# Performance work log

Measured on AMD Instinct MI355X. Metric: run time of the kernel, lower is better.

## Reference

```python
import jax, jax.numpy as jnp
import numpy as np

N = 50000      # nodes
E = 1600000    # edges (avg degree 32)
D_IN = 32
D_EF = 16
D_H = 64
D_MSG = 32
D_UP = 32


def setup_inputs() -> dict:
    key = jax.random.key(0)
    ks = jax.random.split(key, 10)
    s = 0.05
    return {
        "x": jax.random.normal(ks[0], (N, D_IN), dtype=jnp.float32),
        "degrees": jax.random.uniform(ks[1], (N, 1), dtype=jnp.float32),
        "edge_features": jax.random.normal(ks[2], (E, D_EF), dtype=jnp.float32),
        "W1m": jax.random.normal(ks[3], (2 * D_IN + D_EF, D_H), dtype=jnp.float32) * s,
        "b1m": jnp.zeros((D_H,), dtype=jnp.float32),
        "W2m": jax.random.normal(ks[4], (D_H, D_MSG), dtype=jnp.float32) * s,
        "b2m": jnp.zeros((D_MSG,), dtype=jnp.float32),
        "W1u": jax.random.normal(ks[5], (D_IN + D_MSG, D_H), dtype=jnp.float32) * s,
        "b1u": jnp.zeros((D_H,), dtype=jnp.float32),
        "W2u": jax.random.normal(ks[6], (D_H, D_UP), dtype=jnp.float32) * s,
        "b2u": jnp.zeros((D_UP,), dtype=jnp.float32),
        "edge_index": jax.random.randint(ks[7], (2, E), 0, N, dtype=jnp.int64),
    }


def mlp2(h, W1, b1, W2, b2):
    return jax.nn.relu(h @ W1 + b1) @ W2 + b2


def reference(x, degrees, edge_features, W1m, b1m, W2m, b2m, W1u, b1u, W2u, b2u, edge_index):
    # flow = 'source_to_target': select=1 -> i = targets = edge_index[1],
    # j = sources = edge_index[0]; sparse.sum over dim 0 aggregates per target.
    src = edge_index[0]
    dst = edge_index[1]
    x_i = x[dst]                                  # [E, D_IN] target features
    x_j = x[src]                                  # [E, D_IN] source features
    msg_in = jnp.concatenate([x_i, x_j, edge_features], axis=-1)  # [E, 2*D_IN+D_EF]
    msgs = mlp2(msg_in, W1m, b1m, W2m, b2m)       # [E, D_MSG]
    agg = jax.ops.segment_sum(msgs, dst, num_segments=x.shape[0])  # [N, D_MSG]
    upd_in = jnp.concatenate([x, agg], axis=-1)   # [N, D_IN+D_MSG]
    return mlp2(upd_in, W1u, b1u, W2u, b2u)       # [N, D_UP]
```

## Files before the change

### kernel.cpp

```cpp
#include <hip/hip_runtime.h>
#include <hip/hip_bf16.h>

#define D_IN  32
#define D_EF  16
#define D_H   64
#define D_MSG 32
#define D_UP  32

typedef __fp16 v2h __attribute__((ext_vector_type(2)));

__device__ __forceinline__ unsigned bf16pair(float a, float b) {
    unsigned ua = __float_as_uint(a);
    ua = (ua + 0x7fffu + ((ua >> 16) & 1u)) >> 16;
    unsigned ub = __float_as_uint(b);
    ub = (ub + 0x7fffu + ((ub >> 16) & 1u)) >> 16;
    return ua | (ub << 16);
}
__device__ __forceinline__ float bf_lo(unsigned u) { return __uint_as_float(u << 16); }
__device__ __forceinline__ float bf_hi(unsigned u) { return __uint_as_float(u & 0xffff0000u); }

__global__ __launch_bounds__(256) void prep_kernel(
    const float* __restrict__ x,
    const float* __restrict__ W1m,
    const float* __restrict__ b1m,
    const int*   __restrict__ ei,
    float* __restrict__ P1,
    unsigned short* __restrict__ P2b,
    int* __restrict__ deg,
    int* __restrict__ rank,
    v2h* __restrict__ W1Ep,
    int n_nodes, int n_edges, int NBn, int NBe)
{
    int b = blockIdx.x;

    if (b < NBn) {
        int i = b * 256 + threadIdx.x;
        if (i >= n_nodes) return;

        float xi[D_IN];
        const float4* xp = (const float4*)(x + (size_t)i * D_IN);
#pragma unroll
        for (int k4 = 0; k4 < D_IN / 4; ++k4) {
            float4 v = xp[k4];
            xi[4 * k4 + 0] = v.x; xi[4 * k4 + 1] = v.y;
            xi[4 * k4 + 2] = v.z; xi[4 * k4 + 3] = v.w;
        }
        {
            float acc[D_H];
#pragma unroll
            for (int j = 0; j < D_H; ++j) acc[j] = b1m[j];
            for (int k = 0; k < D_IN; ++k) {
                float xv = xi[k];
                const float* wr = W1m + (size_t)k * D_H;
#pragma unroll
                for (int j = 0; j < D_H; ++j) acc[j] += xv * wr[j];
            }
            float4* o = (float4*)(P1 + (size_t)i * D_H);
#pragma unroll
            for (int j4 = 0; j4 < D_H / 4; ++j4)
                o[j4] = make_float4(acc[4 * j4], acc[4 * j4 + 1],
                                    acc[4 * j4 + 2], acc[4 * j4 + 3]);
        }
        {
            float acc[D_H];
#pragma unroll
            for (int j = 0; j < D_H; ++j) acc[j] = 0.0f;
            for (int k = 0; k < D_IN; ++k) {
                float xv = xi[k];
                const float* wr = W1m + (size_t)(k + D_IN) * D_H;
#pragma unroll
                for (int j = 0; j < D_H; ++j) acc[j] += xv * wr[j];
            }
            uint4* o = (uint4*)(P2b + (size_t)i * D_H);
#pragma unroll
            for (int j8 = 0; j8 < D_H / 8; ++j8) {
                uint4 q;
                q.x = bf16pair(acc[8 * j8 + 0], acc[8 * j8 + 1]);
                q.y = bf16pair(acc[8 * j8 + 2], acc[8 * j8 + 3]);
                q.z = bf16pair(acc[8 * j8 + 4], acc[8 * j8 + 5]);
                q.w = bf16pair(acc[8 * j8 + 6], acc[8 * j8 + 7]);
                o[j8] = q;
            }
        }
    } else if (b < NBn + NBe) {
        int e = (b - NBn) * 256 + threadIdx.x;
        if (e < n_edges)
            rank[e] = atomicAdd(&deg[ei[n_edges + e]], 1);
    } else {
        int t = threadIdx.x;
        const float* W1E = W1m + (size_t)(2 * D_IN) * D_H;
        for (int idx = t; idx < 8 * D_H; idx += 256) {
            int kp = idx >> 6, c = idx & 63;
            W1Ep[idx] = __builtin_amdgcn_cvt_pkrtz(W1E[(2 * kp) * D_H + c],
                                                   W1E[(2 * kp + 1) * D_H + c]);
        }
    }
}

__global__ __launch_bounds__(256) void scan_partials_kernel(
    const int* __restrict__ deg, int* __restrict__ bsum, int n_nodes)
{
    int idx = blockIdx.x * 256 + threadIdx.x;
    int v = (idx < n_nodes) ? deg[idx] : 0;
#pragma unroll
    for (int o = 1; o < 64; o <<= 1) v += __shfl_xor(v, o, 64);
    __shared__ int ws[4];
    int lane = threadIdx.x & 63, w = threadIdx.x >> 6;
    if (lane == 0) ws[w] = v;
    __syncthreads();
    if (threadIdx.x == 0) bsum[blockIdx.x] = ws[0] + ws[1] + ws[2] + ws[3];
}

__global__ __launch_bounds__(256) void scan_blockoffs_kernel(
    const int* __restrict__ bsum, int* __restrict__ boffs, int nb)
{
    __shared__ int sdata[256];
    int t = threadIdx.x;
    sdata[t] = (t < nb) ? bsum[t] : 0;
    __syncthreads();
    for (int off = 1; off < 256; off <<= 1) {
        int u = (t >= off) ? sdata[t - off] : 0;
        __syncthreads();
        sdata[t] += u;
        __syncthreads();
    }
    if (t < nb) boffs[t] = (t > 0) ? sdata[t - 1] : 0;
}

__global__ __launch_bounds__(256) void scan_final_kernel(
    const int* __restrict__ deg, const int* __restrict__ boffs,
    int* __restrict__ offs, int n_nodes)
{
    __shared__ int sdata[256];
    int t = threadIdx.x;
    int idx = blockIdx.x * 256 + t;
    sdata[t] = (idx < n_nodes) ? deg[idx] : 0;
    __syncthreads();
    for (int off = 1; off < 256; off <<= 1) {
        int u = (t >= off) ? sdata[t - off] : 0;
        __syncthreads();
        sdata[t] += u;
        __syncthreads();
    }
    int excl = boffs[blockIdx.x] + ((t > 0) ? sdata[t - 1] : 0);
    if (idx < n_nodes) offs[idx] = excl;
}

__global__ __launch_bounds__(256) void scatter_kernel(
    const int* __restrict__ ei,
    const int* __restrict__ rank,
    const int* __restrict__ offs,
    int2* __restrict__ edges_sorted,
    int n_edges)
{
    int e = blockIdx.x * blockDim.x + threadIdx.x;
    if (e < n_edges) {
        int s = ei[e];
        int d = ei[n_edges + e];
        int pos = offs[d] + rank[e];
        edges_sorted[pos] = make_int2(e, s);
    }
}

__global__ __launch_bounds__(256) void gather_kernel(
    const float* __restrict__ ef,
    const v2h*  __restrict__ W1Ep,
    const float* __restrict__ P1,
    const unsigned short* __restrict__ P2b,
    const int*  __restrict__ deg,
    const int*  __restrict__ offs,
    const int2* __restrict__ edges_sorted,
    float* __restrict__ hagg,
    int n_nodes)
{
    int tid = blockIdx.x * blockDim.x + threadIdx.x;
    int n = tid >> 4;
    int t = tid & 15;
    if (n >= n_nodes) return;

    int start = offs[n];
    int end   = start + deg[n];
    const float* P1n = P1 + (size_t)n * D_H;

    float hacc[D_H];
#pragma unroll
    for (int c = 0; c < D_H; ++c) hacc[c] = 0.0f;

    int i = start + t;
    int s = 0;
    float4 ef0, ef1, ef2, ef3;
    if (i < end) {
        int2 es = edges_sorted[i];
        s = es.y;
        const float4* efp = (const float4*)(ef + (size_t)es.x * D_EF);
        ef0 = efp[0]; ef1 = efp[1]; ef2 = efp[2]; ef3 = efp[3];
    }

    while (i < end) {
        int inext = i + 16;
        int ip = (inext < end) ? inext : i;
        int2 es2 = edges_sorted[ip];
        const float4* efp2 = (const float4*)(ef + (size_t)es2.x * D_EF);
        float4 nf0 = efp2[0], nf1 = efp2[1], nf2 = efp2[2], nf3 = efp2[3];

        v2h efh[D_EF / 2];
        efh[0] = __builtin_amdgcn_cvt_pkrtz(ef0.x, ef0.y);
        efh[1] = __builtin_amdgcn_cvt_pkrtz(ef0.z, ef0.w);
        efh[2] = __builtin_amdgcn_cvt_pkrtz(ef1.x, ef1.y);
        efh[3] = __builtin_amdgcn_cvt_pkrtz(ef1.z, ef1.w);
        efh[4] = __builtin_amdgcn_cvt_pkrtz(ef2.x, ef2.y);
        efh[5] = __builtin_amdgcn_cvt_pkrtz(ef2.z, ef2.w);
        efh[6] = __builtin_amdgcn_cvt_pkrtz(ef3.x, ef3.y);
        efh[7] = __builtin_amdgcn_cvt_pkrtz(ef3.z, ef3.w);

        const float4* p1  = (const float4*)P1n;
        const uint4*  p2u = (const uint4*)(P2b + (size_t)s * D_H);

#pragma unroll
        for (int j = 0; j < D_H / 8; ++j) {
            uint4 b = p2u[j];
            float4 a0 = p1[2 * j], a1 = p1[2 * j + 1];
            float h[8];
            h[0] = a0.x + bf_lo(b.x); h[1] = a0.y + bf_hi(b.x);
            h[2] = a0.z + bf_lo(b.y); h[3] = a0.w + bf_hi(b.y);
            h[4] = a1.x + bf_lo(b.z); h[5] = a1.y + bf_hi(b.z);
            h[6] = a1.z + bf_lo(b.w); h[7] = a1.w + bf_hi(b.w);

#pragma unroll
            for (int kp = 0; kp < D_EF / 2; ++kp) {
                const v2h* wr = W1Ep + kp * D_H + 8 * j;
#pragma unroll
                for (int c8 = 0; c8 < 8; ++c8)
                    h[c8] = __builtin_amdgcn_fdot2(efh[kp], wr[c8], h[c8], false);
            }

#pragma unroll
            for (int c8 = 0; c8 < 8; ++c8) {
                float r = h[c8] > 0.0f ? h[c8] : 0.0f;
                hacc[8 * j + c8] += r;
            }
        }

        i = inext; s = es2.y;
        ef0 = nf0; ef1 = nf1; ef2 = nf2; ef3 = nf3;
    }

    float r1[32];
    {
        const bool up = (t & 8) != 0;
#pragma unroll
        for (int c = 0; c < 32; ++c) {
            float lo = hacc[c]      + __shfl_xor(hacc[c],      8, 16);
            float hi = hacc[c + 32] + __shfl_xor(hacc[c + 32], 8, 16);
            r1[c] = up ? hi : lo;
        }
    }
    float r2[16];
    {
        const bool up = (t & 4) != 0;
#pragma unroll
        for (int c = 0; c < 16; ++c) {
            float lo = r1[c]      + __shfl_xor(r1[c],      4, 16);
            float hi = r1[c + 16] + __shfl_xor(r1[c + 16], 4, 16);
            r2[c] = up ? hi : lo;
        }
    }
    float r3[8];
    {
        const bool up = (t & 2) != 0;
#pragma unroll
        for (int c = 0; c < 8; ++c) {
            float lo = r2[c]     + __shfl_xor(r2[c],     2, 16);
            float hi = r2[c + 8] + __shfl_xor(r2[c + 8], 2, 16);
            r3[c] = up ? hi : lo;
        }
    }
    float r4[4];
    {
        const bool up = (t & 1) != 0;
#pragma unroll
        for (int c = 0; c < 4; ++c) {
            float lo = r3[c]     + __shfl_xor(r3[c],     1, 16);
            float hi = r3[c + 4] + __shfl_xor(r3[c + 4], 1, 16);
            r4[c] = up ? hi : lo;
        }
    }

    ((float4*)(hagg + (size_t)n * D_H))[t] =
        make_float4(r4[0], r4[1], r4[2], r4[3]);
}

__global__ __launch_bounds__(256) void node_upd_kernel(
    const float* __restrict__ x,
    const float* __restrict__ hagg,
    const int*   __restrict__ deg,
    const float* __restrict__ b2m,
    const float* __restrict__ W2m,
    const float* __restrict__ W1u,
    const float* __restrict__ b1u,
    const float* __restrict__ W2u,
    const float* __restrict__ b2u,
    float* __restrict__ out,
    int n_nodes)
{
    int i = blockIdx.x * blockDim.x + threadIdx.x;
    if (i >= n_nodes) return;

    float in[D_IN + D_MSG];
    const float4* xp = (const float4*)(x + (size_t)i * D_IN);
#pragma unroll
    for (int k4 = 0; k4 < D_IN / 4; ++k4) {
        float4 v = xp[k4];
        in[4 * k4 + 0] = v.x; in[4 * k4 + 1] = v.y;
        in[4 * k4 + 2] = v.z; in[4 * k4 + 3] = v.w;
    }

    float dc = (float)deg[i];
#pragma unroll
    for (int m = 0; m < D_MSG; ++m) in[D_IN + m] = dc * b2m[m];

    const float4* hp = (const float4*)(hagg + (size_t)i * D_H);
    for (int j4 = 0; j4 < D_H / 4; ++j4) {
        float4 v = hp[j4];
        const float* w0 = W2m + (size_t)(4 * j4 + 0) * D_MSG;
        const float* w1 = W2m + (size_t)(4 * j4 + 1) * D_MSG;
        const float* w2 = W2m + (size_t)(4 * j4 + 2) * D_MSG;
        const float* w3 = W2m + (size_t)(4 * j4 + 3) * D_MSG;
#pragma unroll
        for (int m = 0; m < D_MSG; ++m)
            in[D_IN + m] += v.x * w0[m] + v.y * w1[m] + v.z * w2[m] + v.w * w3[m];
    }

    float h[D_H];
#pragma unroll
    for (int j = 0; j < D_H; ++j) h[j] = b1u[j];
    for (int k = 0; k < D_IN + D_MSG; ++k) {
        float v = in[k];
        const float* wr = W1u + (size_t)k * D_H;
#pragma unroll
        for (int j = 0; j < D_H; ++j) h[j] += v * wr[j];
    }

    float o[D_UP];
#pragma unroll
    for (int m = 0; m < D_UP; ++m) o[m] = b2u[m];
    for (int j = 0; j < D_H; ++j) {
        float r = h[j] > 0.0f ? h[j] : 0.0f;
        const float* wr = W2u + (size_t)j * D_UP;
#pragma unroll
        for (int m = 0; m < D_UP; ++m) o[m] += r * wr[m];
    }

    float4* op = (float4*)(out + (size_t)i * D_UP);
#pragma unroll
    for (int m4 = 0; m4 < D_UP / 4; ++m4)
        op[m4] = make_float4(o[4 * m4], o[4 * m4 + 1], o[4 * m4 + 2], o[4 * m4 + 3]);
}

extern "C" void kernel_launch(void* const* d_in, const int* in_sizes, int n_in,
                              void* d_out, int out_size, void* d_ws, size_t ws_size,
                              hipStream_t stream) {
    const float* x    = (const float*)d_in[0];
    const float* ef   = (const float*)d_in[2];
    const float* W1m  = (const float*)d_in[3];
    const float* b1m  = (const float*)d_in[4];
    const float* W2m  = (const float*)d_in[5];
    const float* b2m  = (const float*)d_in[6];
    const float* W1u  = (const float*)d_in[7];
    const float* b1u  = (const float*)d_in[8];
    const float* W2u  = (const float*)d_in[9];
    const float* b2u  = (const float*)d_in[10];
    const int*   ei   = (const int*)d_in[11];

    const int n_nodes = in_sizes[0] / D_IN;
    const int n_edges = in_sizes[11] / 2;

    float* out = (float*)d_out;

    const int NBn = (n_nodes + 255) / 256;
    const int NBe = (n_edges + 255) / 256;

    float*          P1  = (float*)d_ws;
    unsigned short* P2b = (unsigned short*)(P1 + (size_t)n_nodes * D_H);
    int2* edges_sorted  = (int2*)(P2b + (size_t)n_nodes * D_H);
    int* deg    = (int*)(edges_sorted + n_edges);
    int* offs   = deg    + n_nodes;
    int* bsum   = offs   + n_nodes;
    int* boffs  = bsum   + NBn;
    v2h* W1Ep   = (v2h*)(boffs + NBn);
    int*   rank = (int*)(W1Ep + 8 * D_H);
    float* hagg = (float*)rank;

    hipMemsetAsync(deg, 0, (size_t)n_nodes * sizeof(int), stream);

    prep_kernel<<<NBn + NBe + 1, 256, 0, stream>>>(
        x, W1m, b1m, ei, P1, P2b, deg, rank, W1Ep,
        n_nodes, n_edges, NBn, NBe);

    scan_partials_kernel<<<NBn, 256, 0, stream>>>(deg, bsum, n_nodes);
    scan_blockoffs_kernel<<<1, 256, 0, stream>>>(bsum, boffs, NBn);
    scan_final_kernel<<<NBn, 256, 0, stream>>>(deg, boffs, offs, n_nodes);

    scatter_kernel<<<NBe, 256, 0, stream>>>(ei, rank, offs, edges_sorted, n_edges);

    {
        long total = (long)n_nodes * 16;
        int grid = (int)((total + 255) / 256);
        gather_kernel<<<grid, 256, 0, stream>>>(ef, W1Ep, P1, P2b,
                                                deg, offs, edges_sorted, hagg,
                                                n_nodes);
    }
    node_upd_kernel<<<NBn, 256, 0, stream>>>(x, hagg, deg, b2m, W2m,
                                             W1u, b1u, W2u, b2u, out, n_nodes);
}
```

Measured before the change: 516.5 us.

## Split gather hidden channels across four waves per node group

Each 256-thread block now handles 4 nodes. Each wavefront covers one 16-column slice of the 64-wide hidden layer, so a thread keeps 16 accumulators instead of 64. The point is to cut register pressure, raise occupancy (launch bounds of 6 waves) and shrink the shuffle reduction. The cost is that every wave re-reads edges_sorted and the edge features, so those reads rise 4x, and the software prefetch of the next edge is gone.

```diff
diff --git a/kernel.cpp b/kernel.cpp
--- a/kernel.cpp
+++ b/kernel.cpp
@@ -162,7 +162,7 @@
     }
 }
 
-__global__ __launch_bounds__(256) void gather_kernel(
+__global__ __launch_bounds__(256, 6) void gather_kernel(
     const float* __restrict__ ef,
     const v2h*  __restrict__ W1Ep,
     const float* __restrict__ P1,
@@ -173,62 +173,66 @@
     float* __restrict__ hagg,
     int n_nodes)
 {
-    int tid = blockIdx.x * blockDim.x + threadIdx.x;
-    int n = tid >> 4;
-    int t = tid & 15;
+    const int lane = threadIdx.x & 63;
+    const int cg   = __builtin_amdgcn_readfirstlane((int)(threadIdx.x >> 6));
+    const int g    = lane >> 4;
+    const int t    = lane & 15;
+    const int n    = blockIdx.x * 4 + g;
     if (n >= n_nodes) return;
 
-    int start = offs[n];
-    int end   = start + deg[n];
-    const float* P1n = P1 + (size_t)n * D_H;
-
-    float hacc[D_H];
-#pragma unroll
-    for (int c = 0; c < D_H; ++c) hacc[c] = 0.0f;
-
-    int i = start + t;
-    int s = 0;
-    float4 ef0, ef1, ef2, ef3;
-    if (i < end) {
+    const int start = offs[n];
+    const int end   = start + deg[n];
+
+    float p1q[16];
+    {
+        const float4* pp = (const float4*)(P1 + (size_t)n * D_H + cg * 16);
+#pragma unroll
+        for (int q = 0; q < 4; ++q) {
+            float4 v = pp[q];
+            p1q[4 * q + 0] = v.x; p1q[4 * q + 1] = v.y;
+            p1q[4 * q + 2] = v.z; p1q[4 * q + 3] = v.w;
+        }
+    }
+
+    const v2h* wbase = W1Ep + 16 * cg;
+
+    float hacc[16];
+#pragma unroll
+    for (int c = 0; c < 16; ++c) hacc[c] = 0.0f;
+
+    for (int i = start + t; i < end; i += 16) {
         int2 es = edges_sorted[i];
-        s = es.y;
         const float4* efp = (const float4*)(ef + (size_t)es.x * D_EF);
-        ef0 = efp[0]; ef1 = efp[1]; ef2 = efp[2]; ef3 = efp[3];
-    }
-
-    while (i < end) {
-        int inext = i + 16;
-        int ip = (inext < end) ? inext : i;
-        int2 es2 = edges_sorted[ip];
-        const float4* efp2 = (const float4*)(ef + (size_t)es2.x * D_EF);
-        float4 nf0 = efp2[0], nf1 = efp2[1], nf2 = efp2[2], nf3 = efp2[3];
+        float4 f0 = efp[0], f1 = efp[1], f2 = efp[2], f3 = efp[3];
+        const uint4* p2u = (const uint4*)(P2b + (size_t)es.y * D_H + cg * 16);
+        uint4 b0 = p2u[0], b1 = p2u[1];
 
         v2h efh[D_EF / 2];
-        efh[0] = __builtin_amdgcn_cvt_pkrtz(ef0.x, ef0.y);
-        efh[1] = __builtin_amdgcn_cvt_pkrtz(ef0.z, ef0.w);
-        efh[2] = __builtin_amdgcn_cvt_pkrtz(ef1.x, ef1.y);
-        efh[3] = __builtin_amdgcn_cvt_pkrtz(ef1.z, ef1.w);
-        efh[4] = __builtin_amdgcn_cvt_pkrtz(ef2.x, ef2.y);
-        efh[5] = __builtin_amdgcn_cvt_pkrtz(ef2.z, ef2.w);
-        efh[6] = __builtin_amdgcn_cvt_pkrtz(ef3.x, ef3.y);
-        efh[7] = __builtin_amdgcn_cvt_pkrtz(ef3.z, ef3.w);
-
-        const float4* p1  = (const float4*)P1n;
-        const uint4*  p2u = (const uint4*)(P2b + (size_t)s * D_H);
-
-#pragma unroll
-        for (int j = 0; j < D_H / 8; ++j) {
-            uint4 b = p2u[j];
-            float4 a0 = p1[2 * j], a1 = p1[2 * j + 1];
+        efh[0] = __builtin_amdgcn_cvt_pkrtz(f0.x, f0.y);
+        efh[1] = __builtin_amdgcn_cvt_pkrtz(f0.z, f0.w);
+        efh[2] = __builtin_amdgcn_cvt_pkrtz(f1.x, f1.y);
+        efh[3] = __builtin_amdgcn_cvt_pkrtz(f1.z, f1.w);
+        efh[4] = __builtin_amdgcn_cvt_pkrtz(f2.x, f2.y);
+        efh[5] = __builtin_amdgcn_cvt_pkrtz(f2.z, f2.w);
+        efh[6] = __builtin_amdgcn_cvt_pkrtz(f3.x, f3.y);
+        efh[7] = __builtin_amdgcn_cvt_pkrtz(f3.z, f3.w);
+
+#pragma unroll
+        for (int jj = 0; jj < 2; ++jj) {
+            uint4 b = jj ? b1 : b0;
             float h[8];
-            h[0] = a0.x + bf_lo(b.x); h[1] = a0.y + bf_hi(b.x);
-            h[2] = a0.z + bf_lo(b.y); h[3] = a0.w + bf_hi(b.y);
-            h[4] = a1.x + bf_lo(b.z); h[5] = a1.y + bf_hi(b.z);
-            h[6] = a1.z + bf_lo(b.w); h[7] = a1.w + bf_hi(b.w);
+            h[0] = p1q[8 * jj + 0] + bf_lo(b.x);
+            h[1] = p1q[8 * jj + 1] + bf_hi(b.x);
+            h[2] = p1q[8 * jj + 2] + bf_lo(b.y);
+            h[3] = p1q[8 * jj + 3] + bf_hi(b.y);
+            h[4] = p1q[8 * jj + 4] + bf_lo(b.z);
+            h[5] = p1q[8 * jj + 5] + bf_hi(b.z);
+            h[6] = p1q[8 * jj + 6] + bf_lo(b.w);
+            h[7] = p1q[8 * jj + 7] + bf_hi(b.w);
 
 #pragma unroll
             for (int kp = 0; kp < D_EF / 2; ++kp) {
-                const v2h* wr = W1Ep + kp * D_H + 8 * j;
+                const v2h* wr = wbase + kp * D_H + 8 * jj;
 #pragma unroll
                 for (int c8 = 0; c8 < 8; ++c8)
                     h[c8] = __builtin_amdgcn_fdot2(efh[kp], wr[c8], h[c8], false);
@@ -237,57 +241,50 @@
 #pragma unroll
             for (int c8 = 0; c8 < 8; ++c8) {
                 float r = h[c8] > 0.0f ? h[c8] : 0.0f;
-                hacc[8 * j + c8] += r;
+                hacc[8 * jj + c8] += r;
             }
         }
-
-        i = inext; s = es2.y;
-        ef0 = nf0; ef1 = nf1; ef2 = nf2; ef3 = nf3;
-    }
-
-    float r1[32];
+    }
+
+    float r1[8];
     {
         const bool up = (t & 8) != 0;
 #pragma unroll
-        for (int c = 0; c < 32; ++c) {
-            float lo = hacc[c]      + __shfl_xor(hacc[c],      8, 16);
-            float hi = hacc[c + 32] + __shfl_xor(hacc[c + 32], 8, 16);
+        for (int c = 0; c < 8; ++c) {
+            float lo = hacc[c]     + __shfl_xor(hacc[c],     8, 16);
+            float hi = hacc[c + 8] + __shfl_xor(hacc[c + 8], 8, 16);
             r1[c] = up ? hi : lo;
         }
     }
-    float r2[16];
+    float r2[4];
     {
         const bool up = (t & 4) != 0;
 #pragma unroll
-        for (int c = 0; c < 16; ++c) {
-            float lo = r1[c]      + __shfl_xor(r1[c],      4, 16);
-            float hi = r1[c + 16] + __shfl_xor(r1[c + 16], 4, 16);
+        for (int c = 0; c < 4; ++c) {
+            float lo = r1[c]     + __shfl_xor(r1[c],     4, 16);
+            float hi = r1[c + 4] + __shfl_xor(r1[c + 4], 4, 16);
             r2[c] = up ? hi : lo;
         }
     }
-    float r3[8];
+    float r3[2];
     {
         const bool up = (t & 2) != 0;
 #pragma unroll
-        for (int c = 0; c < 8; ++c) {
+        for (int c = 0; c < 2; ++c) {
             float lo = r2[c]     + __shfl_xor(r2[c],     2, 16);
-            float hi = r2[c + 8] + __shfl_xor(r2[c + 8], 2, 16);
+            float hi = r2[c + 2] + __shfl_xor(r2[c + 2], 2, 16);
             r3[c] = up ? hi : lo;
         }
     }
-    float r4[4];
+    float r4;
     {
         const bool up = (t & 1) != 0;
-#pragma unroll
-        for (int c = 0; c < 4; ++c) {
-            float lo = r3[c]     + __shfl_xor(r3[c],     1, 16);
-            float hi = r3[c + 4] + __shfl_xor(r3[c + 4], 1, 16);
-            r4[c] = up ? hi : lo;
-        }
-    }
-
-    ((float4*)(hagg + (size_t)n * D_H))[t] =
-        make_float4(r4[0], r4[1], r4[2], r4[3]);
+        float lo = r3[0] + __shfl_xor(r3[0], 1, 16);
+        float hi = r3[1] + __shfl_xor(r3[1], 1, 16);
+        r4 = up ? hi : lo;
+    }
+
+    hagg[(size_t)n * D_H + cg * 16 + t] = r4;
 }
 
 __global__ __launch_bounds__(256) void node_upd_kernel(
@@ -404,8 +401,7 @@
     scatter_kernel<<<NBe, 256, 0, stream>>>(ei, rank, offs, edges_sorted, n_edges);
 
     {
-        long total = (long)n_nodes * 16;
-        int grid = (int)((total + 255) / 256);
+        int grid = (n_nodes + 3) / 4;
         gather_kernel<<<grid, 256, 0, stream>>>(ef, W1Ep, P1, P2b,
                                                 deg, offs, edges_sorted, hagg,
                                                 n_nodes);
```

Measured after the change: 450.0 us. 1.15x faster.
